# Optimization experiments

Hardware: AMD Instinct MI355X
Metric: run time of the kernel (lower is better)

The kernel has to match this reference:

```python
import jax, jax.numpy as jnp
import numpy as np
from jax import lax

WINS = [3, 5, 7, 11, 15, 19]
MAXW = 19
PAD = MAXW // 2 + 1          # 10, matches F.pad(..., max_wh//2+1)
NEG_HALF = (-MAXW) // 2      # -10, matches torch's `-self.max_wh // 2` (floor div)
EPS_IN = 1e-5
EPS_DEV = 1e-6


def _conv(x, w, b, dil):
    # x: [B,C,H,W], w: [O,I,kh,kw], 'same' padding with dilation
    y = lax.conv_general_dilated(x, w, (1, 1), 'SAME',
                                 rhs_dilation=(dil, dil),
                                 dimension_numbers=('NCHW', 'OIHW', 'NCHW'))
    return y + b[None, :, None, None]


def _inorm_relu(y):
    # InstanceNorm2d(affine=False): per-sample per-channel over H,W, biased var
    m = jnp.mean(y, axis=(2, 3), keepdims=True)
    v = jnp.mean((y - m) ** 2, axis=(2, 3), keepdims=True)
    return jax.nn.relu((y - m) * lax.rsqrt(v + EPS_IN))


def _integral(x):
    # x: [B,H,W,C] -> padded double cumsum (integral image) [B,H+2P,W+2P,C]
    xp = jnp.pad(x, ((0, 0), (PAD, PAD), (PAD, PAD), (0, 0)))
    return jnp.cumsum(jnp.cumsum(xp, axis=1), axis=2)


def _box_sum(ii, h, w):
    # 4-corner integral-image lookup; slices reproduce torch offsets exactly
    top = MAXW // 2 - h // 2
    bot = top + h
    left = MAXW // 2 - w // 2
    right = left + w
    top0 = NEG_HALF - h // 2 - 1
    bot0 = top0 + h
    left0 = NEG_HALF - w // 2 - 1
    right0 = left0 + w
    return (ii[:, top:top0, left:left0] + ii[:, bot:bot0, right:right0]
            - ii[:, top:top0, right:right0] - ii[:, bot:bot0, left:left0])


def _multi_window_mean(x):
    # x: [B,H,W,1] -> [B,n_wins,H,W,1] of window means
    ii = _integral(x)
    cnt_ii = _integral(jnp.ones_like(x[:1]))  # [1,...] pixel-count integral
    means = [_box_sum(ii, hw, hw) / _box_sum(cnt_ii, hw, hw) for hw in WINS]
    return jnp.stack(means, axis=1)


def _sauvola(x1, k, R):
    E_x = _multi_window_mean(x1)
    E_x2 = _multi_window_mean(x1 * x1)
    dev = jnp.sqrt(jnp.maximum(E_x2 - E_x ** 2, EPS_DEV))
    return E_x * (1.0 + k * (dev / R - 1.0))  # [B,n,H,W,1]


def setup_inputs() -> dict:
    key = jax.random.key(0)
    ks = jax.random.split(key, 16)
    B, H, W = 4, 768, 768
    base = 4
    chans = [1, 4, 8, 12, 16, 20, 24]
    d = {'x': jax.random.uniform(ks[0], (B, 1, H, W), dtype=jnp.float32)}
    names = ['conv1', 'convs1', 'convs2', 'convs3', 'convs4', 'convs5']
    for i, nm in enumerate(names):
        cin, cout = chans[i], chans[i + 1]
        d[nm + '_w'] = jax.random.normal(ks[1 + i], (cout, cin, 3, 3), dtype=jnp.float32) * 0.1
        d[nm + '_b'] = jax.random.normal(ks[7 + i], (cout,), dtype=jnp.float32) * 0.01
    d['conv2_w'] = jax.random.normal(ks[13], (len(WINS), 24, 3, 3), dtype=jnp.float32) * 0.1
    d['conv2_b'] = jax.random.normal(ks[14], (len(WINS),), dtype=jnp.float32) * 0.01
    d['k'] = jnp.full((1, len(WINS), 1, 1, 1), 0.2, dtype=jnp.float32)
    d['R'] = jnp.full((1, len(WINS), 1, 1, 1), 0.5, dtype=jnp.float32)
    d['alpha'] = jnp.full((1, 1, 1, 1), 16.0, dtype=jnp.float32)
    return d


def reference(x, conv1_w, conv1_b, convs1_w, convs1_b, convs2_w, convs2_b,
              convs3_w, convs3_b, convs4_w, convs4_b, convs5_w, convs5_b,
              conv2_w, conv2_b, k, R, alpha):
    y = _inorm_relu(_conv(x, conv1_w, conv1_b, 1))
    for w, b in ((convs1_w, convs1_b), (convs2_w, convs2_b), (convs3_w, convs3_b),
                 (convs4_w, convs4_b), (convs5_w, convs5_b)):
        y = _inorm_relu(_conv(y, w, b, 2))
    f = jax.nn.softmax(_conv(y, conv2_w, conv2_b, 1), axis=1)  # [B,n,H,W]
    x1 = jnp.transpose(x, (0, 2, 3, 1))                        # [B,H,W,1]
    th = _sauvola(x1, k, R)                                    # [B,n,H,W,1]
    th1 = jnp.sum(f[..., None] * th, axis=1)                   # [B,H,W,1]
    diff = (x1 - th1) * alpha / (1.0 - 0.0)                    # img_range (0,1)
    return jnp.transpose(diff, (0, 3, 1, 2))                   # [B,1,H,W]
```

## Files before the change

kernel.cpp:

```cpp
#include <hip/hip_runtime.h>
#include <math.h>

#define BDIM 256
typedef __bf16 bf16;
typedef __bf16 bf16x4 __attribute__((ext_vector_type(4)));
typedef __bf16 bf16x8 __attribute__((ext_vector_type(8)));
typedef float f32x4 __attribute__((ext_vector_type(4)));
typedef float f32x2 __attribute__((ext_vector_type(2)));

template <bool V> struct BC { static constexpr bool value = V; };

constexpr int B_ = 4, H_ = 768, W_ = 768;
constexpr int HW_ = H_ * W_;
constexpr int TS = 16;
constexpr int NTB = W_ / TS;
constexpr int NBLK = HW_ / (TS * TS);

constexpr int PMAX_FLOATS = 4 * NBLK * 48;
constexpr int OUT_ELEMS   = B_ * HW_;

__device__ void repack_one(const float* __restrict__ src, bf16* __restrict__ dst,
                           int CIN, int CINP, int COUT, int NT16, int KPP)
{
    const int n_ = NT16 * KPP;
    for (int idx = threadIdx.x; idx < n_; idx += BDIM) {
        const int n = idx / KPP, k = idx - n * KPP;
        const int tap = k / CINP, ci = k - tap * CINP;
        float v = 0.f;
        if (n < COUT && tap < 9 && ci < CIN)
            v = src[(n * CIN + ci) * 9 + tap];
        dst[idx] = (bf16)v;
    }
}

__global__ __launch_bounds__(BDIM) void repack_all(
    const float* w0, const float* w1, const float* w2, const float* w3,
    const float* w4, const float* w5, const float* wf,
    bf16* r0, bf16* r1, bf16* r2, bf16* r3, bf16* r4, bf16* r5, bf16* rf)
{
    switch (blockIdx.x) {
        case 0: repack_one(w0, r0, 1,  8,  4,  16, 104); break;
        case 1: repack_one(w1, r1, 4,  8,  8,  16, 104); break;
        case 2: repack_one(w2, r2, 8,  8,  12, 16, 104); break;
        case 3: repack_one(w3, r3, 12, 16, 16, 16, 168); break;
        case 4: repack_one(w4, r4, 16, 16, 20, 32, 168); break;
        case 5: repack_one(w5, r5, 20, 24, 24, 32, 232); break;
        case 6: repack_one(wf, rf, 24, 24, 6,  16, 232); break;
    }
}

template <int CIN, int CINP, int COUT, int DIL, bool FIRST>
__global__ __launch_bounds__(BDIM) void conv_mfma(
    const void* __restrict__ inv,
    const float* __restrict__ prevStats,
    const bf16* __restrict__ wp,
    const float* __restrict__ bias,
    bf16* __restrict__ y,
    float* __restrict__ partials)
{
    constexpr int TW = TS + 2 * DIL;
    constexpr int KP = ((9 * CINP + 31) / 32) * 32;
    constexpr int KPP = KP + 8;
    constexpr int NT = (COUT + 15) / 16;
    constexpr int KS = KP / 32;
    constexpr int CSTR = (CINP == 16) ? 24 : CINP;
    __shared__ __align__(16) bf16 tile[TW * TW * CSTR];
    __shared__ float sred[4][2 * COUT];

    const int s = blockIdx.x / NBLK;
    const int blk = blockIdx.x - s * NBLK;
    const int ti = blk / NTB, tj = blk - ti * NTB;
    const int i0 = ti * TS - DIL, j0 = tj * TS - DIL;
    const int t = threadIdx.x;
    const bool interior = (i0 >= 0) & (j0 >= 0) &
                          (i0 + TW <= H_) & (j0 + TW <= W_);

    const float* ps = prevStats + s * 2 * CIN;
    auto stage = [&](auto bc) {
        constexpr bool IN = decltype(bc)::value;
        for (int loc = t; loc < TW * TW; loc += BDIM) {
            const int rr = loc / TW, cc = loc - rr * TW;
            const int gi = i0 + rr, gj = j0 + cc;
            bool ok = true;
            if constexpr (!IN)
                ok = (gi >= 0) & (gi < H_) & (gj >= 0) & (gj < W_);
            float lv[CSTR];
#pragma unroll
            for (int c = 0; c < CSTR; ++c) lv[c] = 0.f;
            if (ok) {
                if constexpr (FIRST) {
                    const float* xg = (const float*)inv + (size_t)s * HW_;
                    lv[0] = xg[(size_t)gi * W_ + gj];
                } else {
                    const bf16* ing = (const bf16*)inv +
                                      ((size_t)s * HW_ + (size_t)gi * W_ + gj) * CIN;
                    if constexpr (CIN % 8 == 0) {
#pragma unroll
                        for (int qq = 0; qq < CIN / 8; ++qq) {
                            bf16x8 raw = ((const bf16x8*)ing)[qq];
#pragma unroll
                            for (int u = 0; u < 8; ++u) {
                                const int ci = 8 * qq + u;
                                lv[ci] = fmaxf(fmaf((float)raw[u], ps[2 * ci], ps[2 * ci + 1]), 0.f);
                            }
                        }
                    } else {
#pragma unroll
                        for (int qq = 0; qq < CIN / 4; ++qq) {
                            bf16x4 raw = ((const bf16x4*)ing)[qq];
#pragma unroll
                            for (int u = 0; u < 4; ++u) {
                                const int ci = 4 * qq + u;
                                lv[ci] = fmaxf(fmaf((float)raw[u], ps[2 * ci], ps[2 * ci + 1]), 0.f);
                            }
                        }
                    }
                }
            }
            bf16* lp = tile + loc * CSTR;
#pragma unroll
            for (int g = 0; g < CSTR / 8; ++g) {
                bf16x8 pk;
#pragma unroll
                for (int u = 0; u < 8; ++u) pk[u] = (bf16)lv[8 * g + u];
                *(bf16x8*)(lp + 8 * g) = pk;
            }
        }
    };
    if (interior) stage(BC<true>{}); else stage(BC<false>{});
    __syncthreads();

    const int wave = t >> 6, lane = t & 63, q = lane >> 4, ln = lane & 15;
    f32x4 acc[4][NT];
#pragma unroll
    for (int mt = 0; mt < 4; ++mt)
#pragma unroll
        for (int u = 0; u < NT; ++u) acc[mt][u] = (f32x4){0.f, 0.f, 0.f, 0.f};

    auto aOff = [&](int ks) -> int {
        int k0 = ks * 32 + q * 8;
        int tap = k0 / CINP;
        int ci0 = k0 - tap * CINP;
        if (tap > 8) { tap = 0; ci0 = 0; }
        const int ky = tap / 3, kx = tap - 3 * ky;
        return (ky * DIL * TW + kx * DIL) * CSTR + ci0;
    };

    bf16x8 bfr[NT], bfrN[NT];
    bf16x8 af[4], afN[4];
#pragma unroll
    for (int u = 0; u < NT; ++u)
        bfr[u] = *(const bf16x8*)&wp[(u * 16 + ln) * KPP + q * 8];
    {
        const int ao = aOff(0);
#pragma unroll
        for (int mt = 0; mt < 4; ++mt)
            af[mt] = *(const bf16x8*)&tile[((wave * 4 + mt) * TW + ln) * CSTR + ao];
    }

#pragma unroll
    for (int ks = 0; ks < KS; ++ks) {
        if (ks + 1 < KS) {
#pragma unroll
            for (int u = 0; u < NT; ++u)
                bfrN[u] = *(const bf16x8*)&wp[(u * 16 + ln) * KPP + (ks + 1) * 32 + q * 8];
            const int ao = aOff(ks + 1);
#pragma unroll
            for (int mt = 0; mt < 4; ++mt)
                afN[mt] = *(const bf16x8*)&tile[((wave * 4 + mt) * TW + ln) * CSTR + ao];
        }
#pragma unroll
        for (int mt = 0; mt < 4; ++mt)
#pragma unroll
            for (int u = 0; u < NT; ++u)
                acc[mt][u] = __builtin_amdgcn_mfma_f32_16x16x32_bf16(
                    af[mt], bfr[u], acc[mt][u], 0, 0, 0);
#pragma unroll
        for (int u = 0; u < NT; ++u) bfr[u] = bfrN[u];
#pragma unroll
        for (int mt = 0; mt < 4; ++mt) af[mt] = afN[mt];
    }

#pragma unroll
    for (int u = 0; u < NT; ++u) {
        const int n = u * 16 + ln;
        const float bv = (n < COUT) ? bias[n] : 0.f;
        float s1 = 0.f, s2 = 0.f;
#pragma unroll
        for (int mt = 0; mt < 4; ++mt)
#pragma unroll
            for (int r = 0; r < 4; ++r) {
                const float v = acc[mt][u][r] + bv;
                acc[mt][u][r] = v;
                s1 += v; s2 += v * v;
            }
        s1 += __shfl_xor(s1, 16); s1 += __shfl_xor(s1, 32);
        s2 += __shfl_xor(s2, 16); s2 += __shfl_xor(s2, 32);
        if (lane < 16 && n < COUT) { sred[wave][n] = s1; sred[wave][COUT + n] = s2; }
    }
    __syncthreads();
    if (t < 2 * COUT) {
        partials[((size_t)s * NBLK + blk) * (2 * COUT) + t] =
            sred[0][t] + sred[1][t] + sred[2][t] + sred[3][t];
    }

    bf16* ost = tile;
#pragma unroll
    for (int u = 0; u < NT; ++u) {
        const int n = u * 16 + ln;
        if (n < COUT) {
#pragma unroll
            for (int mt = 0; mt < 4; ++mt)
#pragma unroll
                for (int r = 0; r < 4; ++r) {
                    const int pl = (wave * 4 + mt) * 16 + q * 4 + r;
                    ost[pl * COUT + n] = (bf16)acc[mt][u][r];
                }
        }
    }
    __syncthreads();

    const int lr = t >> 4, lc = t & 15;
    bf16* yp = y + (size_t)s * HW_ * COUT +
               ((size_t)(ti * TS + lr) * W_ + (tj * TS + lc)) * COUT;
    const bf16* sp = ost + t * COUT;
    if constexpr (COUT % 8 == 0) {
#pragma unroll
        for (int g = 0; g < COUT / 8; ++g)
            ((bf16x8*)yp)[g] = ((const bf16x8*)sp)[g];
    } else {
#pragma unroll
        for (int g = 0; g < COUT / 4; ++g)
            ((bf16x4*)yp)[g] = ((const bf16x4*)sp)[g];
    }
}

template <int COUT>
__global__ __launch_bounds__(BDIM) void reduce_stats(
    const float* __restrict__ partials, float* __restrict__ stats)
{
    const int s = blockIdx.x / COUT;
    const int co = blockIdx.x - s * COUT;
    const float* P = partials + (size_t)s * NBLK * (2 * COUT);
    float s1 = 0.f, s2 = 0.f;
    for (int k = threadIdx.x; k < NBLK; k += BDIM) {
        const float* p = P + (size_t)k * (2 * COUT);
        s1 += p[co];
        s2 += p[COUT + co];
    }
#pragma unroll
    for (int off = 32; off; off >>= 1) {
        s1 += __shfl_xor(s1, off);
        s2 += __shfl_xor(s2, off);
    }
    __shared__ float l1[4], l2[4];
    const int lane = threadIdx.x & 63, wave = threadIdx.x >> 6;
    if (lane == 0) { l1[wave] = s1; l2[wave] = s2; }
    __syncthreads();
    if (threadIdx.x == 0) {
        float t1 = l1[0] + l1[1] + l1[2] + l1[3];
        float t2 = l2[0] + l2[1] + l2[2] + l2[3];
        float m = t1 / (float)HW_;
        float var = t2 / (float)HW_ - m * m;
        const float rs = rsqrtf(var + 1e-5f);
        stats[((size_t)s * COUT + co) * 2 + 0] = rs;
        stats[((size_t)s * COUT + co) * 2 + 1] = -m * rs;
    }
}

__global__ __launch_bounds__(BDIM) void conv2_sauvola(
    const bf16* __restrict__ in, const float* __restrict__ prevStats,
    const bf16* __restrict__ wp, const float* __restrict__ bias,
    const float* __restrict__ x,
    const float* __restrict__ kArr, const float* __restrict__ RArr,
    const float* __restrict__ alphaP, float* __restrict__ outp)
{
    constexpr int CIN = 24, CINP = 24, COUT = 6, DIL = 1;
    constexpr int TW = TS + 2 * DIL;
    constexpr int KPP = 232, KS = 7, CSTR = 24;
    constexpr int R9 = 9;
    constexpr int TSW = TS + 2 * R9;
    constexpr int ISTR = 37;
    constexpr int SLOG_STR = 7;
    __shared__ __align__(16) bf16 tile[TW * TW * CSTR];
    __shared__ __align__(16) f32x2 I12[35 * ISTR];

    const int s = blockIdx.x / NBLK;
    const int blk = blockIdx.x - s * NBLK;
    const int ti = blk / NTB, tj = blk - ti * NTB;
    const int i0 = ti * TS - DIL, j0 = tj * TS - DIL;
    const int is0 = ti * TS - R9, js0 = tj * TS - R9;
    const int t = threadIdx.x;
    const float* xs = x + (size_t)s * HW_;
    const bool interior = (is0 >= 0) & (js0 >= 0) &
                          (is0 + TSW <= H_) & (js0 + TSW <= W_);

    const float* ps = prevStats + s * 2 * CIN;
    auto stage = [&](auto bc) {
        constexpr bool IN = decltype(bc)::value;
        for (int loc = t; loc < TW * TW; loc += BDIM) {
            const int rr = loc / TW, cc = loc - rr * TW;
            const int gi = i0 + rr, gj = j0 + cc;
            bool ok = true;
            if constexpr (!IN)
                ok = (gi >= 0) & (gi < H_) & (gj >= 0) & (gj < W_);
            float lv[CSTR];
#pragma unroll
            for (int c = 0; c < CSTR; ++c) lv[c] = 0.f;
            if (ok) {
                const bf16* ing = in + ((size_t)s * HW_ + (size_t)gi * W_ + gj) * CIN;
#pragma unroll
                for (int qq = 0; qq < CIN / 8; ++qq) {
                    bf16x8 raw = ((const bf16x8*)ing)[qq];
#pragma unroll
                    for (int u = 0; u < 8; ++u) {
                        const int ci = 8 * qq + u;
                        lv[ci] = fmaxf(fmaf((float)raw[u], ps[2 * ci], ps[2 * ci + 1]), 0.f);
                    }
                }
            }
            bf16* lp = tile + loc * CSTR;
#pragma unroll
            for (int g = 0; g < CSTR / 8; ++g) {
                bf16x8 pk;
#pragma unroll
                for (int u = 0; u < 8; ++u) pk[u] = (bf16)lv[8 * g + u];
                *(bf16x8*)(lp + 8 * g) = pk;
            }
        }
        for (int loc = t; loc < TSW * TSW; loc += BDIM) {
            const int rr = loc / TSW, cc = loc - rr * TSW;
            const int gi = is0 + rr, gj = js0 + cc;
            float v;
            if constexpr (IN) {
                v = xs[(size_t)gi * W_ + gj];
            } else {
                v = 0.f;
                if ((gi >= 0) & (gi < H_) & (gj >= 0) & (gj < W_))
                    v = xs[(size_t)gi * W_ + gj];
            }
            I12[(rr + 1) * ISTR + cc + 1] = (f32x2){v, v * v};
        }
    };
    if (interior) stage(BC<true>{}); else stage(BC<false>{});
    for (int idx = t; idx < 35 + 34; idx += BDIM) {
        if (idx < 35) I12[idx] = (f32x2){0.f, 0.f};
        else I12[(idx - 35 + 1) * ISTR] = (f32x2){0.f, 0.f};
    }
    __syncthreads();

    const int wave = t >> 6, lane = t & 63, q = lane >> 4, ln = lane & 15;
    f32x4 acc[4];
#pragma unroll
    for (int mt = 0; mt < 4; ++mt) acc[mt] = (f32x4){0.f, 0.f, 0.f, 0.f};

    auto aOff = [&](int ks) -> int {
        int k0 = ks * 32 + q * 8;
        int tap = k0 / CINP;
        int ci0 = k0 - tap * CINP;
        if (tap > 8) { tap = 0; ci0 = 0; }
        const int ky = tap / 3, kx = tap - 3 * ky;
        return (ky * DIL * TW + kx * DIL) * CSTR + ci0;
    };

    bf16x8 bfr, bfrN;
    bf16x8 af[4], afN[4];
    bfr = *(const bf16x8*)&wp[ln * KPP + q * 8];
    {
        const int ao = aOff(0);
#pragma unroll
        for (int mt = 0; mt < 4; ++mt)
            af[mt] = *(const bf16x8*)&tile[((wave * 4 + mt) * TW + ln) * CSTR + ao];
    }
#pragma unroll
    for (int ks = 0; ks < KS; ++ks) {
        if (ks + 1 < KS) {
            bfrN = *(const bf16x8*)&wp[ln * KPP + (ks + 1) * 32 + q * 8];
            const int ao = aOff(ks + 1);
#pragma unroll
            for (int mt = 0; mt < 4; ++mt)
                afN[mt] = *(const bf16x8*)&tile[((wave * 4 + mt) * TW + ln) * CSTR + ao];
        }
#pragma unroll
        for (int mt = 0; mt < 4; ++mt)
            acc[mt] = __builtin_amdgcn_mfma_f32_16x16x32_bf16(af[mt], bfr, acc[mt], 0, 0, 0);
        bfr = bfrN;
#pragma unroll
        for (int mt = 0; mt < 4; ++mt) af[mt] = afN[mt];
    }
    __syncthreads();

    float* slog = (float*)tile;
    const float bv = (ln < COUT) ? bias[ln] : 0.f;
#pragma unroll
    for (int mt = 0; mt < 4; ++mt)
#pragma unroll
        for (int r = 0; r < 4; ++r)
            if (ln < COUT) {
                const int pl = (wave * 4 + mt) * 16 + q * 4 + r;
                slog[pl * SLOG_STR + ln] = acc[mt][r] + bv;
            }
    if (t < 34) {
        f32x2* row = I12 + (t + 1) * ISTR;
        f32x2 a = (f32x2){0.f, 0.f};
#pragma unroll 2
        for (int c = 1; c <= TSW; ++c) { a += row[c]; row[c] = a; }
    }
    __syncthreads();

    if (t < 34) {
        const int c = t + 1;
        f32x2 a = (f32x2){0.f, 0.f};
#pragma unroll 2
        for (int r = 1; r <= TSW; ++r) {
            f32x2* p = &I12[r * ISTR + c];
            a += *p; *p = a;
        }
    }
    float e[COUT];
    {
        float mx = slog[t * SLOG_STR];
#pragma unroll
        for (int co = 1; co < COUT; ++co) mx = fmaxf(mx, slog[t * SLOG_STR + co]);
        float sm = 0.f;
#pragma unroll
        for (int co = 0; co < COUT; ++co) { e[co] = __expf(slog[t * SLOG_STR + co] - mx); sm += e[co]; }
        const float inv = 1.f / sm;
#pragma unroll
        for (int co = 0; co < COUT; ++co) e[co] *= inv;
    }
    float c0w[6], c1w[6];
#pragma unroll
    for (int wi = 0; wi < 6; ++wi) {
        const float kk = kArr[wi], rr = RArr[wi];
        c0w[wi] = kk / rr;
        c1w[wi] = 1.f - kk;
    }
    const int lr = t >> 4, lc = t & 15;
    const int gi = ti * TS + lr, gj = tj * TS + lc;
    const float xv = xs[(size_t)gi * W_ + gj];
    const float alpha = alphaP[0];
    __syncthreads();

    const int wins[6] = {3, 5, 7, 11, 15, 19};
    const float invc_tab[6] = {1.f / 9.f,  1.f / 25.f,  1.f / 49.f,
                               1.f / 121.f, 1.f / 225.f, 1.f / 361.f};
    float th1 = 0.f;
    if (interior) {
#pragma unroll
        for (int wi = 0; wi < 6; ++wi) {
            const int r = wins[wi] >> 1;
            const float invc = invc_tab[wi];
            const int top = lr + R9 - r, bot = lr + R9 + r + 1;
            const int lef = lc + R9 - r, rig = lc + R9 + r + 1;
            const f32x2 Atl = I12[top * ISTR + lef];
            const f32x2 Atr = I12[top * ISTR + rig];
            const f32x2 Abl = I12[bot * ISTR + lef];
            const f32x2 Abr = I12[bot * ISTR + rig];
            const f32x2 sm2 = Abr - Atr - Abl + Atl;
            const float Ex = sm2.x * invc;
            const float Ex2 = sm2.y * invc;
            const float dev = sqrtf(fmaxf(Ex2 - Ex * Ex, 1e-6f));
            const float th = Ex * fmaf(dev, c0w[wi], c1w[wi]);
            th1 = fmaf(e[wi], th, th1);
        }
    } else {
#pragma unroll
        for (int wi = 0; wi < 6; ++wi) {
            const int r = wins[wi] >> 1;
            const int r0 = max(gi - r, 0), r1i = min(gi + r, H_ - 1);
            const int c0 = max(gj - r, 0), c1 = min(gj + r, W_ - 1);
            const float invc = 1.f / (float)((r1i - r0 + 1) * (c1 - c0 + 1));
            const int top = lr + R9 - r, bot = lr + R9 + r + 1;
            const int lef = lc + R9 - r, rig = lc + R9 + r + 1;
            const f32x2 Atl = I12[top * ISTR + lef];
            const f32x2 Atr = I12[top * ISTR + rig];
            const f32x2 Abl = I12[bot * ISTR + lef];
            const f32x2 Abr = I12[bot * ISTR + rig];
            const f32x2 sm2 = Abr - Atr - Abl + Atl;
            const float Ex = sm2.x * invc;
            const float Ex2 = sm2.y * invc;
            const float dev = sqrtf(fmaxf(Ex2 - Ex * Ex, 1e-6f));
            const float th = Ex * fmaf(dev, c0w[wi], c1w[wi]);
            th1 = fmaf(e[wi], th, th1);
        }
    }
    outp[(size_t)s * HW_ + (size_t)gi * W_ + gj] = (xv - th1) * alpha;
}

extern "C" void kernel_launch(void* const* d_in, const int* in_sizes, int n_in,
                              void* d_out, int out_size, void* d_ws, size_t ws_size,
                              hipStream_t stream) {
    const float* x   = (const float*)d_in[0];
    const float* w0  = (const float*)d_in[1];  const float* b0 = (const float*)d_in[2];
    const float* w1  = (const float*)d_in[3];  const float* b1 = (const float*)d_in[4];
    const float* w2  = (const float*)d_in[5];  const float* b2 = (const float*)d_in[6];
    const float* w3  = (const float*)d_in[7];  const float* b3 = (const float*)d_in[8];
    const float* w4  = (const float*)d_in[9];  const float* b4 = (const float*)d_in[10];
    const float* w5  = (const float*)d_in[11]; const float* b5 = (const float*)d_in[12];
    const float* wf  = (const float*)d_in[13]; const float* bf = (const float*)d_in[14];
    const float* kA  = (const float*)d_in[15];
    const float* RA  = (const float*)d_in[16];
    const float* alp = (const float*)d_in[17];
    float* out = (float*)d_out;
    (void)n_in; (void)in_sizes; (void)out_size;

    float* partials = out + (OUT_ELEMS - PMAX_FLOATS - 256);
    float* stats    = out + (OUT_ELEMS - 224);

    auto need = [](int nb) -> size_t {
        size_t o = 0;
        auto al = [&](size_t bytes) { o += (bytes + 255) & ~(size_t)255; };
        al((size_t)nb * HW_ * 20 * 2);
        al((size_t)nb * HW_ * 24 * 2);
        al(1664 * 2); al(1664 * 2); al(1664 * 2); al(2688 * 2);
        al(5376 * 2); al(7424 * 2); al(3712 * 2);
        return o;
    };
    int nb = 1;
    if (ws_size >= need(4)) nb = 4;
    else if (ws_size >= need(2)) nb = 2;

    char* ws = (char*)d_ws;
    size_t off = 0;
    auto alloc = [&](size_t bytes) -> void* {
        void* p = ws + off;
        off += (bytes + 255) & ~(size_t)255;
        return p;
    };
    bf16*  bufA = (bf16*)alloc((size_t)nb * HW_ * 20 * 2);
    bf16*  bufB = (bf16*)alloc((size_t)nb * HW_ * 24 * 2);
    bf16* r0 = (bf16*)alloc(1664 * 2);
    bf16* r1 = (bf16*)alloc(1664 * 2);
    bf16* r2 = (bf16*)alloc(1664 * 2);
    bf16* r3 = (bf16*)alloc(2688 * 2);
    bf16* r4 = (bf16*)alloc(5376 * 2);
    bf16* r5 = (bf16*)alloc(7424 * 2);
    bf16* rf = (bf16*)alloc(3712 * 2);

    const dim3 blk(BDIM);
    const int cg = nb * NBLK;

    repack_all<<<7, blk, 0, stream>>>(w0, w1, w2, w3, w4, w5, wf,
                                      r0, r1, r2, r3, r4, r5, rf);

    for (int it = 0; it < B_ / nb; ++it) {
        const float* xc   = x   + (size_t)it * nb * HW_;
        float*       outc = out + (size_t)it * nb * HW_;

        conv_mfma<1, 8, 4, 1, true><<<cg, blk, 0, stream>>>(xc, nullptr, r0, b0, bufA, partials);
        reduce_stats<4><<<nb * 4, blk, 0, stream>>>(partials, stats);

        conv_mfma<4, 8, 8, 2, false><<<cg, blk, 0, stream>>>(bufA, stats, r1, b1, bufB, partials);
        reduce_stats<8><<<nb * 8, blk, 0, stream>>>(partials, stats);

        conv_mfma<8, 8, 12, 2, false><<<cg, blk, 0, stream>>>(bufB, stats, r2, b2, bufA, partials);
        reduce_stats<12><<<nb * 12, blk, 0, stream>>>(partials, stats);

        conv_mfma<12, 16, 16, 2, false><<<cg, blk, 0, stream>>>(bufA, stats, r3, b3, bufB, partials);
        reduce_stats<16><<<nb * 16, blk, 0, stream>>>(partials, stats);

        conv_mfma<16, 16, 20, 2, false><<<cg, blk, 0, stream>>>(bufB, stats, r4, b4, bufA, partials);
        reduce_stats<20><<<nb * 20, blk, 0, stream>>>(partials, stats);

        conv_mfma<20, 24, 24, 2, false><<<cg, blk, 0, stream>>>(bufA, stats, r5, b5, bufB, partials);
        reduce_stats<24><<<nb * 24, blk, 0, stream>>>(partials, stats);

        conv2_sauvola<<<cg, blk, 0, stream>>>(
            bufB, stats, rf, bf, xc, kA, RA, alp, outc);
    }
}
```

Measured before the change: 405.4 us.

## Enlarge final conv+Sauvola tile to 32x32 and transpose partial-stat layout

The final conv2+Sauvola kernel now processes 32x32 output tiles with 512 threads, each thread handling two pixels and each wave eight MFMA row tiles. This cuts the relative halo overhead of the 19x19 window integral image and the conv halo. Separately, the per-block instance-norm partials are stored channel-major so reduce_stats reads them contiguously instead of with a stride. The change drops the register-level prefetch in the MFMA loop and raises shared memory use per block, which may reduce occupancy.

After: 404.6 us. About the same (-0.2%).

```diff
diff --git a/kernel.cpp b/kernel.cpp
--- a/kernel.cpp
+++ b/kernel.cpp
@@ -2,6 +2,7 @@
 #include <math.h>
 
 #define BDIM 256
+#define BDIM2 512
 typedef __bf16 bf16;
 typedef __bf16 bf16x4 __attribute__((ext_vector_type(4)));
 typedef __bf16 bf16x8 __attribute__((ext_vector_type(8)));
@@ -15,6 +16,9 @@
 constexpr int TS = 16;
 constexpr int NTB = W_ / TS;
 constexpr int NBLK = HW_ / (TS * TS);
+constexpr int TS2 = 32;
+constexpr int NTB2 = W_ / TS2;
+constexpr int NBLK2 = HW_ / (TS2 * TS2);
 
 constexpr int PMAX_FLOATS = 4 * NBLK * 48;
 constexpr int OUT_ELEMS   = B_ * HW_;
@@ -56,7 +60,8 @@
     const bf16* __restrict__ wp,
     const float* __restrict__ bias,
     bf16* __restrict__ y,
-    float* __restrict__ partials)
+    float* __restrict__ partials,
+    int NBT)
 {
     constexpr int TW = TS + 2 * DIL;
     constexpr int KP = ((9 * CINP + 31) / 32) * 32;
@@ -200,7 +205,7 @@
     }
     __syncthreads();
     if (t < 2 * COUT) {
-        partials[((size_t)s * NBLK + blk) * (2 * COUT) + t] =
+        partials[(size_t)t * NBT + (size_t)s * NBLK + blk] =
             sred[0][t] + sred[1][t] + sred[2][t] + sred[3][t];
     }
 
@@ -237,16 +242,16 @@
 
 template <int COUT>
 __global__ __launch_bounds__(BDIM) void reduce_stats(
-    const float* __restrict__ partials, float* __restrict__ stats)
+    const float* __restrict__ partials, float* __restrict__ stats, int NBT)
 {
     const int s = blockIdx.x / COUT;
     const int co = blockIdx.x - s * COUT;
-    const float* P = partials + (size_t)s * NBLK * (2 * COUT);
+    const float* P1 = partials + (size_t)co * NBT + (size_t)s * NBLK;
+    const float* P2 = partials + (size_t)(COUT + co) * NBT + (size_t)s * NBLK;
     float s1 = 0.f, s2 = 0.f;
     for (int k = threadIdx.x; k < NBLK; k += BDIM) {
-        const float* p = P + (size_t)k * (2 * COUT);
-        s1 += p[co];
-        s2 += p[COUT + co];
+        s1 += P1[k];
+        s2 += P2[k];
     }
 #pragma unroll
     for (int off = 32; off; off >>= 1) {
@@ -268,28 +273,28 @@
     }
 }
 
-__global__ __launch_bounds__(BDIM) void conv2_sauvola(
+__global__ __launch_bounds__(BDIM2) void conv2_sauvola(
     const bf16* __restrict__ in, const float* __restrict__ prevStats,
     const bf16* __restrict__ wp, const float* __restrict__ bias,
     const float* __restrict__ x,
     const float* __restrict__ kArr, const float* __restrict__ RArr,
     const float* __restrict__ alphaP, float* __restrict__ outp)
 {
-    constexpr int CIN = 24, CINP = 24, COUT = 6, DIL = 1;
-    constexpr int TW = TS + 2 * DIL;
+    constexpr int CIN = 24, CINP = 24, COUT = 6;
+    constexpr int TW = TS2 + 2;
     constexpr int KPP = 232, KS = 7, CSTR = 24;
     constexpr int R9 = 9;
-    constexpr int TSW = TS + 2 * R9;
-    constexpr int ISTR = 37;
+    constexpr int TSW = TS2 + 2 * R9;
+    constexpr int ISTR = 51;
     constexpr int SLOG_STR = 7;
     __shared__ __align__(16) bf16 tile[TW * TW * CSTR];
-    __shared__ __align__(16) f32x2 I12[35 * ISTR];
-
-    const int s = blockIdx.x / NBLK;
-    const int blk = blockIdx.x - s * NBLK;
-    const int ti = blk / NTB, tj = blk - ti * NTB;
-    const int i0 = ti * TS - DIL, j0 = tj * TS - DIL;
-    const int is0 = ti * TS - R9, js0 = tj * TS - R9;
+    __shared__ __align__(16) f32x2 I12[(TSW + 1) * ISTR];
+
+    const int s = blockIdx.x / NBLK2;
+    const int blk = blockIdx.x - s * NBLK2;
+    const int ti = blk / NTB2, tj = blk - ti * NTB2;
+    const int i0 = ti * TS2 - 1, j0 = tj * TS2 - 1;
+    const int is0 = ti * TS2 - R9, js0 = tj * TS2 - R9;
     const int t = threadIdx.x;
     const float* xs = x + (size_t)s * HW_;
     const bool interior = (is0 >= 0) & (js0 >= 0) &
@@ -298,7 +303,7 @@
     const float* ps = prevStats + s * 2 * CIN;
     auto stage = [&](auto bc) {
         constexpr bool IN = decltype(bc)::value;
-        for (int loc = t; loc < TW * TW; loc += BDIM) {
+        for (int loc = t; loc < TW * TW; loc += BDIM2) {
             const int rr = loc / TW, cc = loc - rr * TW;
             const int gi = i0 + rr, gj = j0 + cc;
             bool ok = true;
@@ -328,7 +333,7 @@
                 *(bf16x8*)(lp + 8 * g) = pk;
             }
         }
-        for (int loc = t; loc < TSW * TSW; loc += BDIM) {
+        for (int loc = t; loc < TSW * TSW; loc += BDIM2) {
             const int rr = loc / TSW, cc = loc - rr * TSW;
             const int gi = is0 + rr, gj = js0 + cc;
             float v;
@@ -343,16 +348,16 @@
         }
     };
     if (interior) stage(BC<true>{}); else stage(BC<false>{});
-    for (int idx = t; idx < 35 + 34; idx += BDIM) {
-        if (idx < 35) I12[idx] = (f32x2){0.f, 0.f};
-        else I12[(idx - 35 + 1) * ISTR] = (f32x2){0.f, 0.f};
+    for (int idx = t; idx < (TSW + 1) + TSW; idx += BDIM2) {
+        if (idx < TSW + 1) I12[idx] = (f32x2){0.f, 0.f};
+        else I12[(idx - (TSW + 1) + 1) * ISTR] = (f32x2){0.f, 0.f};
     }
     __syncthreads();
 
     const int wave = t >> 6, lane = t & 63, q = lane >> 4, ln = lane & 15;
-    f32x4 acc[4];
-#pragma unroll
-    for (int mt = 0; mt < 4; ++mt) acc[mt] = (f32x4){0.f, 0.f, 0.f, 0.f};
+    f32x4 acc[8];
+#pragma unroll
+    for (int mt = 0; mt < 8; ++mt) acc[mt] = (f32x4){0.f, 0.f, 0.f, 0.f};
 
     auto aOff = [&](int ks) -> int {
         int k0 = ks * 32 + q * 8;
@@ -360,47 +365,34 @@
         int ci0 = k0 - tap * CINP;
         if (tap > 8) { tap = 0; ci0 = 0; }
         const int ky = tap / 3, kx = tap - 3 * ky;
-        return (ky * DIL * TW + kx * DIL) * CSTR + ci0;
-    };
-
-    bf16x8 bfr, bfrN;
-    bf16x8 af[4], afN[4];
-    bfr = *(const bf16x8*)&wp[ln * KPP + q * 8];
-    {
-        const int ao = aOff(0);
-#pragma unroll
-        for (int mt = 0; mt < 4; ++mt)
-            af[mt] = *(const bf16x8*)&tile[((wave * 4 + mt) * TW + ln) * CSTR + ao];
-    }
+        return (ky * TW + kx) * CSTR + ci0;
+    };
+
 #pragma unroll
     for (int ks = 0; ks < KS; ++ks) {
-        if (ks + 1 < KS) {
-            bfrN = *(const bf16x8*)&wp[ln * KPP + (ks + 1) * 32 + q * 8];
-            const int ao = aOff(ks + 1);
-#pragma unroll
-            for (int mt = 0; mt < 4; ++mt)
-                afN[mt] = *(const bf16x8*)&tile[((wave * 4 + mt) * TW + ln) * CSTR + ao];
-        }
-#pragma unroll
-        for (int mt = 0; mt < 4; ++mt)
-            acc[mt] = __builtin_amdgcn_mfma_f32_16x16x32_bf16(af[mt], bfr, acc[mt], 0, 0, 0);
-        bfr = bfrN;
-#pragma unroll
-        for (int mt = 0; mt < 4; ++mt) af[mt] = afN[mt];
+        const bf16x8 bfr = *(const bf16x8*)&wp[ln * KPP + ks * 32 + q * 8];
+        const int ao = aOff(ks);
+#pragma unroll
+        for (int mt = 0; mt < 8; ++mt) {
+            const int Mt = wave * 8 + mt;
+            const bf16x8 af = *(const bf16x8*)
+                &tile[(((Mt >> 1)) * TW + (Mt & 1) * 16 + ln) * CSTR + ao];
+            acc[mt] = __builtin_amdgcn_mfma_f32_16x16x32_bf16(af, bfr, acc[mt], 0, 0, 0);
+        }
     }
     __syncthreads();
 
     float* slog = (float*)tile;
     const float bv = (ln < COUT) ? bias[ln] : 0.f;
 #pragma unroll
-    for (int mt = 0; mt < 4; ++mt)
+    for (int mt = 0; mt < 8; ++mt)
 #pragma unroll
         for (int r = 0; r < 4; ++r)
             if (ln < COUT) {
-                const int pl = (wave * 4 + mt) * 16 + q * 4 + r;
+                const int pl = (wave * 8 + mt) * 16 + q * 4 + r;
                 slog[pl * SLOG_STR + ln] = acc[mt][r] + bv;
             }
-    if (t < 34) {
+    if (t < TSW) {
         f32x2* row = I12 + (t + 1) * ISTR;
         f32x2 a = (f32x2){0.f, 0.f};
 #pragma unroll 2
@@ -408,7 +400,7 @@
     }
     __syncthreads();
 
-    if (t < 34) {
+    if (t < TSW) {
         const int c = t + 1;
         f32x2 a = (f32x2){0.f, 0.f};
 #pragma unroll 2
@@ -417,18 +409,20 @@
             a += *p; *p = a;
         }
     }
-    float e[COUT];
-    {
-        float mx = slog[t * SLOG_STR];
-#pragma unroll
-        for (int co = 1; co < COUT; ++co) mx = fmaxf(mx, slog[t * SLOG_STR + co]);
+    float e0[COUT], e1[COUT];
+    auto softmax_of = [&](int p, float* e) {
+        float mx = slog[p * SLOG_STR];
+#pragma unroll
+        for (int co = 1; co < COUT; ++co) mx = fmaxf(mx, slog[p * SLOG_STR + co]);
         float sm = 0.f;
 #pragma unroll
-        for (int co = 0; co < COUT; ++co) { e[co] = __expf(slog[t * SLOG_STR + co] - mx); sm += e[co]; }
+        for (int co = 0; co < COUT; ++co) { e[co] = __expf(slog[p * SLOG_STR + co] - mx); sm += e[co]; }
         const float inv = 1.f / sm;
 #pragma unroll
         for (int co = 0; co < COUT; ++co) e[co] *= inv;
-    }
+    };
+    softmax_of(t, e0);
+    softmax_of(t + BDIM2, e1);
     float c0w[6], c1w[6];
 #pragma unroll
     for (int wi = 0; wi < 6; ++wi) {
@@ -436,56 +430,65 @@
         c0w[wi] = kk / rr;
         c1w[wi] = 1.f - kk;
     }
-    const int lr = t >> 4, lc = t & 15;
-    const int gi = ti * TS + lr, gj = tj * TS + lc;
-    const float xv = xs[(size_t)gi * W_ + gj];
+    const int pr0 = t >> 5, pc0 = t & 31;
+    const int pr1 = pr0 + 16, pc1 = pc0;
+    const int gi0 = ti * TS2 + pr0, gj0 = tj * TS2 + pc0;
+    const int gi1 = ti * TS2 + pr1, gj1 = tj * TS2 + pc1;
+    const float xv0 = xs[(size_t)gi0 * W_ + gj0];
+    const float xv1 = xs[(size_t)gi1 * W_ + gj1];
     const float alpha = alphaP[0];
     __syncthreads();
 
     const int wins[6] = {3, 5, 7, 11, 15, 19};
     const float invc_tab[6] = {1.f / 9.f,  1.f / 25.f,  1.f / 49.f,
                                1.f / 121.f, 1.f / 225.f, 1.f / 361.f};
-    float th1 = 0.f;
-    if (interior) {
-#pragma unroll
-        for (int wi = 0; wi < 6; ++wi) {
-            const int r = wins[wi] >> 1;
-            const float invc = invc_tab[wi];
-            const int top = lr + R9 - r, bot = lr + R9 + r + 1;
-            const int lef = lc + R9 - r, rig = lc + R9 + r + 1;
-            const f32x2 Atl = I12[top * ISTR + lef];
-            const f32x2 Atr = I12[top * ISTR + rig];
-            const f32x2 Abl = I12[bot * ISTR + lef];
-            const f32x2 Abr = I12[bot * ISTR + rig];
-            const f32x2 sm2 = Abr - Atr - Abl + Atl;
-            const float Ex = sm2.x * invc;
-            const float Ex2 = sm2.y * invc;
-            const float dev = sqrtf(fmaxf(Ex2 - Ex * Ex, 1e-6f));
-            const float th = Ex * fmaf(dev, c0w[wi], c1w[wi]);
-            th1 = fmaf(e[wi], th, th1);
-        }
-    } else {
-#pragma unroll
-        for (int wi = 0; wi < 6; ++wi) {
-            const int r = wins[wi] >> 1;
-            const int r0 = max(gi - r, 0), r1i = min(gi + r, H_ - 1);
-            const int c0 = max(gj - r, 0), c1 = min(gj + r, W_ - 1);
-            const float invc = 1.f / (float)((r1i - r0 + 1) * (c1 - c0 + 1));
-            const int top = lr + R9 - r, bot = lr + R9 + r + 1;
-            const int lef = lc + R9 - r, rig = lc + R9 + r + 1;
-            const f32x2 Atl = I12[top * ISTR + lef];
-            const f32x2 Atr = I12[top * ISTR + rig];
-            const f32x2 Abl = I12[bot * ISTR + lef];
-            const f32x2 Abr = I12[bot * ISTR + rig];
-            const f32x2 sm2 = Abr - Atr - Abl + Atl;
-            const float Ex = sm2.x * invc;
-            const float Ex2 = sm2.y * invc;
-            const float dev = sqrtf(fmaxf(Ex2 - Ex * Ex, 1e-6f));
-            const float th = Ex * fmaf(dev, c0w[wi], c1w[wi]);
-            th1 = fmaf(e[wi], th, th1);
-        }
-    }
-    outp[(size_t)s * HW_ + (size_t)gi * W_ + gj] = (xv - th1) * alpha;
+    auto sauv = [&](int pr, int pc, int gi, int gj, const float* e) -> float {
+        float th1 = 0.f;
+        if (interior) {
+#pragma unroll
+            for (int wi = 0; wi < 6; ++wi) {
+                const int r = wins[wi] >> 1;
+                const float invc = invc_tab[wi];
+                const int top = pr + R9 - r, bot = pr + R9 + r + 1;
+                const int lef = pc + R9 - r, rig = pc + R9 + r + 1;
+                const f32x2 Atl = I12[top * ISTR + lef];
+                const f32x2 Atr = I12[top * ISTR + rig];
+                const f32x2 Abl = I12[bot * ISTR + lef];
+                const f32x2 Abr = I12[bot * ISTR + rig];
+                const f32x2 sm2 = Abr - Atr - Abl + Atl;
+                const float Ex = sm2.x * invc;
+                const float Ex2 = sm2.y * invc;
+                const float dev = sqrtf(fmaxf(Ex2 - Ex * Ex, 1e-6f));
+                const float th = Ex * fmaf(dev, c0w[wi], c1w[wi]);
+                th1 = fmaf(e[wi], th, th1);
+            }
+        } else {
+#pragma unroll
+            for (int wi = 0; wi < 6; ++wi) {
+                const int r = wins[wi] >> 1;
+                const int r0 = max(gi - r, 0), r1i = min(gi + r, H_ - 1);
+                const int c0 = max(gj - r, 0), c1 = min(gj + r, W_ - 1);
+                const float invc = 1.f / (float)((r1i - r0 + 1) * (c1 - c0 + 1));
+                const int top = pr + R9 - r, bot = pr + R9 + r + 1;
+                const int lef = pc + R9 - r, rig = pc + R9 + r + 1;
+                const f32x2 Atl = I12[top * ISTR + lef];
+                const f32x2 Atr = I12[top * ISTR + rig];
+                const f32x2 Abl = I12[bot * ISTR + lef];
+                const f32x2 Abr = I12[bot * ISTR + rig];
+                const f32x2 sm2 = Abr - Atr - Abl + Atl;
+                const float Ex = sm2.x * invc;
+                const float Ex2 = sm2.y * invc;
+                const float dev = sqrtf(fmaxf(Ex2 - Ex * Ex, 1e-6f));
+                const float th = Ex * fmaf(dev, c0w[wi], c1w[wi]);
+                th1 = fmaf(e[wi], th, th1);
+            }
+        }
+        return th1;
+    };
+    const float th10 = sauv(pr0, pc0, gi0, gj0, e0);
+    const float th11 = sauv(pr1, pc1, gi1, gj1, e1);
+    outp[(size_t)s * HW_ + (size_t)gi0 * W_ + gj0] = (xv0 - th10) * alpha;
+    outp[(size_t)s * HW_ + (size_t)gi1 * W_ + gj1] = (xv1 - th11) * alpha;
 }
 
 extern "C" void kernel_launch(void* const* d_in, const int* in_sizes, int n_in,
@@ -540,6 +543,7 @@
 
     const dim3 blk(BDIM);
     const int cg = nb * NBLK;
+    const int NBT = nb * NBLK;
 
     repack_all<<<7, blk, 0, stream>>>(w0, w1, w2, w3, w4, w5, wf,
                                       r0, r1, r2, r3, r4, r5, rf);
@@ -548,25 +552,25 @@
         const float* xc   = x   + (size_t)it * nb * HW_;
         float*       outc = out + (size_t)it * nb * HW_;
 
-        conv_mfma<1, 8, 4, 1, true><<<cg, blk, 0, stream>>>(xc, nullptr, r0, b0, bufA, partials);
-        reduce_stats<4><<<nb * 4, blk, 0, stream>>>(partials, stats);
-
-        conv_mfma<4, 8, 8, 2, false><<<cg, blk, 0, stream>>>(bufA, stats, r1, b1, bufB, partials);
-        reduce_stats<8><<<nb * 8, blk, 0, stream>>>(partials, stats);
-
-        conv_mfma<8, 8, 12, 2, false><<<cg, blk, 0, stream>>>(bufB, stats, r2, b2, bufA, partials);
-        reduce_stats<12><<<nb * 12, blk, 0, stream>>>(partials, stats);
-
-        conv_mfma<12, 16, 16, 2, false><<<cg, blk, 0, stream>>>(bufA, stats, r3, b3, bufB, partials);
-        reduce_stats<16><<<nb * 16, blk, 0, stream>>>(partials, stats);
-
-        conv_mfma<16, 16, 20, 2, false><<<cg, blk, 0, stream>>>(bufB, stats, r4, b4, bufA, partials);
-        reduce_stats<20><<<nb * 20, blk, 0, stream>>>(partials, stats);
-
-        conv_mfma<20, 24, 24, 2, false><<<cg, blk, 0, stream>>>(bufA, stats, r5, b5, bufB, partials);
-        reduce_stats<24><<<nb * 24, blk, 0, stream>>>(partials, stats);
-
-        conv2_sauvola<<<cg, blk, 0, stream>>>(
+        conv_mfma<1, 8, 4, 1, true><<<cg, blk, 0, stream>>>(xc, nullptr, r0, b0, bufA, partials, NBT);
+        reduce_stats<4><<<nb * 4, blk, 0, stream>>>(partials, stats, NBT);
+
+        conv_mfma<4, 8, 8, 2, false><<<cg, blk, 0, stream>>>(bufA, stats, r1, b1, bufB, partials, NBT);
+        reduce_stats<8><<<nb * 8, blk, 0, stream>>>(partials, stats, NBT);
+
+        conv_mfma<8, 8, 12, 2, false><<<cg, blk, 0, stream>>>(bufB, stats, r2, b2, bufA, partials, NBT);
+        reduce_stats<12><<<nb * 12, blk, 0, stream>>>(partials, stats, NBT);
+
+        conv_mfma<12, 16, 16, 2, false><<<cg, blk, 0, stream>>>(bufA, stats, r3, b3, bufB, partials, NBT);
+        reduce_stats<16><<<nb * 16, blk, 0, stream>>>(partials, stats, NBT);
+
+        conv_mfma<16, 16, 20, 2, false><<<cg, blk, 0, stream>>>(bufB, stats, r4, b4, bufA, partials, NBT);
+        reduce_stats<20><<<nb * 20, blk, 0, stream>>>(partials, stats, NBT);
+
+        conv_mfma<20, 24, 24, 2, false><<<cg, blk, 0, stream>>>(bufA, stats, r5, b5, bufB, partials, NBT);
+        reduce_stats<24><<<nb * 24, blk, 0, stream>>>(partials, stats, NBT);
+
+        conv2_sauvola<<<nb * NBLK2, dim3(BDIM2), 0, stream>>>(
             bufB, stats, rf, bf, xc, kA, RA, alp, outc);
     }
 }
```
